# Kernel tuning notes

Hardware: AMD Instinct MI355X
Metric: run time of the kernel (lower is better)

## Reference

```python
import jax, jax.numpy as jnp
import numpy as np

N_USER, N_MOVIE, E, H, L = 100000, 20000, 1000000, 64, 2
NEG_SLOPE = 0.2  # PyG GATv2Conv default negative_slope


def _rand_edges(k, n_src, n_dst, e):
    k1, k2 = jax.random.split(k)
    src = jax.random.randint(k1, (e,), 0, n_src, dtype=jnp.int32)
    dst = jax.random.randint(k2, (e,), 0, n_dst, dtype=jnp.int32)
    # ensure no src==dst index collisions so PyG's remove_self_loops is a no-op
    dst = jnp.where(dst == src, (dst + 1) % n_dst, dst)
    return jnp.stack([src, dst])


def setup_inputs() -> dict:
    key = jax.random.key(0)
    ks = jax.random.split(key, 8)
    return {
        "x_user": jax.random.normal(ks[0], (N_USER, H), jnp.float32),
        "x_movie": jax.random.normal(ks[1], (N_MOVIE, H), jnp.float32),
        "edge_u2m": _rand_edges(ks[2], N_USER, N_MOVIE, E),
        "edge_m2u": _rand_edges(ks[3], N_MOVIE, N_USER, E),
        # params stacked as [layer, edge_type, ...]; edge_type 0 = user->movie, 1 = movie->user
        "Wl": jax.random.normal(ks[4], (L, 2, H, H), jnp.float32) / np.sqrt(H).astype(np.float32),
        "bl": jnp.zeros((L, 2, H), jnp.float32),
        "Wr": jax.random.normal(ks[5], (L, 2, H, H), jnp.float32) / np.sqrt(H).astype(np.float32),
        "br": jnp.zeros((L, 2, H), jnp.float32),
        "att": jax.random.normal(ks[6], (L, 2, H), jnp.float32) / np.sqrt(H).astype(np.float32),
        "bias": jnp.zeros((L, 2, H), jnp.float32),
    }


def _segment_softmax(scores, seg, n):
    # numerically-stable softmax over variable-degree dst neighborhoods (PyG softmax)
    m = jax.ops.segment_max(scores, seg, num_segments=n)
    ex = jnp.exp(scores - m[seg])
    s = jax.ops.segment_sum(ex, seg, num_segments=n)
    return ex / (s[seg] + 1e-16)


def _gatv2(x_src, x_dst, edge, Wl, bl, Wr, br, att, bias):
    n_src, n_dst = x_src.shape[0], x_dst.shape[0]
    xl = x_src @ Wl + bl  # [N_src, H]
    xr = x_dst @ Wr + br  # [N_dst, H]
    n_loop = min(n_src, n_dst)  # PyG adds self loops with num_nodes = min(N_src, N_dst)
    loop = jnp.arange(n_loop, dtype=edge.dtype)
    src = jnp.concatenate([edge[0], loop])
    dst = jnp.concatenate([edge[1], loop])
    e = jax.nn.leaky_relu(xl[src] + xr[dst], NEG_SLOPE)  # [E', H] gathered per edge
    score = e @ att  # [E']
    alpha = _segment_softmax(score, dst, n_dst)
    out = jax.ops.segment_sum(xl[src] * alpha[:, None], dst, num_segments=n_dst)
    return out + bias


def reference(x_user, x_movie, edge_u2m, edge_m2u, Wl, bl, Wr, br, att, bias):
    for l in range(L):
        new_movie = _gatv2(x_user, x_movie, edge_u2m,
                           Wl[l, 0], bl[l, 0], Wr[l, 0], br[l, 0], att[l, 0], bias[l, 0])
        new_user = _gatv2(x_movie, x_user, edge_m2u,
                          Wl[l, 1], bl[l, 1], Wr[l, 1], br[l, 1], att[l, 1], bias[l, 1])
        x_movie = jax.nn.selu(new_movie)
        x_user = jax.nn.selu(new_user)
    return x_user, x_movie
```

## Files before the change

kernel.cpp:

```cpp
#include <hip/hip_runtime.h>
#include <hip/hip_fp16.h>
#include <cstdint>

#define H 64
#define EPR 16
#define NB 120

__device__ __forceinline__ float selu_f(float x) {
  const float sc = 1.0507009873554805f;
  const float al = 1.6732632423543772f;
  return x > 0.f ? sc * x : sc * al * (expf(x) - 1.f);
}

__global__ __launch_bounds__(256) void gemm64_dual2(
    const float* __restrict__ Au, const float* __restrict__ Am,
    const float* __restrict__ W0u, const float* __restrict__ b0u,
    const float* __restrict__ W1u, const float* __restrict__ b1u,
    const float* __restrict__ W0m, const float* __restrict__ b0m,
    const float* __restrict__ W1m, const float* __restrict__ b1m,
    __half* __restrict__ C0u, float* __restrict__ C1u,
    __half* __restrict__ C0m, float* __restrict__ C1m,
    int Nu, int Nm, int split) {
  __shared__ float Ws0[64 * 64];
  __shared__ float Ws1[64 * 64];
  __shared__ float As[64][65];
  __shared__ float bs0[64], bs1[64];

  const float *A, *W0, *b0, *W1, *b1;
  __half* C0; float* C1; int N, blk;
  if (blockIdx.x < split) {
    A = Au; W0 = W0u; b0 = b0u; W1 = W1u; b1 = b1u;
    C0 = C0u; C1 = C1u; N = Nu; blk = blockIdx.x;
  } else {
    A = Am; W0 = W0m; b0 = b0m; W1 = W1m; b1 = b1m;
    C0 = C0m; C1 = C1m; N = Nm; blk = blockIdx.x - split;
  }

  const int tid = threadIdx.x;
  for (int i = tid; i < 1024; i += 256) {
    ((float4*)Ws0)[i] = ((const float4*)W0)[i];
    ((float4*)Ws1)[i] = ((const float4*)W1)[i];
  }
  if (tid < 64) { bs0[tid] = b0[tid]; bs1[tid] = b1[tid]; }

  const int row0 = blk * 64;
  for (int i = tid; i < 1024; i += 256) {
    int r = i >> 4, c4 = i & 15;
    int row = row0 + r;
    float4 v = make_float4(0.f, 0.f, 0.f, 0.f);
    if (row < N) v = ((const float4*)(A + (size_t)row * H))[c4];
    As[r][c4 * 4 + 0] = v.x;
    As[r][c4 * 4 + 1] = v.y;
    As[r][c4 * 4 + 2] = v.z;
    As[r][c4 * 4 + 3] = v.w;
  }
  __syncthreads();

  const int g = tid & 3;
  const int r = tid >> 2;
  float a0[16], a1[16];
#pragma unroll
  for (int j = 0; j < 16; ++j) { a0[j] = bs0[g * 16 + j]; a1[j] = bs1[g * 16 + j]; }

  for (int k = 0; k < 64; ++k) {
    float ak = As[r][k];
    const float4* w0r = (const float4*)&Ws0[k * 64 + g * 16];
    const float4* w1r = (const float4*)&Ws1[k * 64 + g * 16];
#pragma unroll
    for (int j4 = 0; j4 < 4; ++j4) {
      float4 w0 = w0r[j4], w1 = w1r[j4];
      a0[j4 * 4 + 0] += ak * w0.x; a0[j4 * 4 + 1] += ak * w0.y;
      a0[j4 * 4 + 2] += ak * w0.z; a0[j4 * 4 + 3] += ak * w0.w;
      a1[j4 * 4 + 0] += ak * w1.x; a1[j4 * 4 + 1] += ak * w1.y;
      a1[j4 * 4 + 2] += ak * w1.z; a1[j4 * 4 + 3] += ak * w1.w;
    }
  }

  const int row = row0 + r;
  if (row < N) {
    unsigned pu[8];
#pragma unroll
    for (int j2 = 0; j2 < 8; ++j2) {
      __half2 t = __floats2half2_rn(a0[2 * j2], a0[2 * j2 + 1]);
      pu[j2] = *(unsigned*)&t;
    }
    uint4* c0 = (uint4*)(C0 + (size_t)row * H + g * 16);
    c0[0] = make_uint4(pu[0], pu[1], pu[2], pu[3]);
    c0[1] = make_uint4(pu[4], pu[5], pu[6], pu[7]);

    float4* c1 = (float4*)(C1 + (size_t)row * H + g * 16);
#pragma unroll
    for (int j4 = 0; j4 < 4; ++j4) {
      c1[j4] = make_float4(a1[j4 * 4 + 0], a1[j4 * 4 + 1], a1[j4 * 4 + 2], a1[j4 * 4 + 3]);
    }
  }
}

__global__ __launch_bounds__(256) void bucket_hist(
    const int* __restrict__ ed1, int E1r, int n1e, int sh1, int B1, int* __restrict__ mat1,
    const int* __restrict__ ed2, int E2r, int n2e, int sh2, int B2, int* __restrict__ mat2) {
  __shared__ int hist[640];
  int b = blockIdx.x;
  const int* ed; int Er, ne, sh, Bn, blk; int* mat;
  if (b < NB) { ed = ed1; Er = E1r; ne = n1e; sh = sh1; Bn = B1; mat = mat1; blk = b; }
  else { ed = ed2; Er = E2r; ne = n2e; sh = sh2; Bn = B2; mat = mat2; blk = b - NB; }
  for (int i = threadIdx.x; i < Bn; i += 256) hist[i] = 0;
  __syncthreads();
  int chunk = (ne + NB - 1) / NB;
  int lo = blk * chunk, hi = lo + chunk;
  if (hi > ne) hi = ne;
  for (int e = lo + threadIdx.x; e < hi; e += 256) {
    int d = (e < Er) ? ed[e] : (e - Er);
    atomicAdd(&hist[d >> sh], 1);
  }
  __syncthreads();
  for (int i = threadIdx.x; i < Bn; i += 256) mat[(size_t)i * NB + blk] = hist[i];
}

__global__ __launch_bounds__(256) void scan_partial2(
    const int* __restrict__ cnt1, int n1, int* __restrict__ psum1, int* __restrict__ bsum1,
    const int* __restrict__ cnt2, int n2, int* __restrict__ psum2, int* __restrict__ bsum2,
    int split) {
  __shared__ int sh[256];
  int b = blockIdx.x;
  const int* cnt; int n; int* psum; int* bsum; int lb;
  if (b < split) { cnt = cnt1; n = n1; psum = psum1; bsum = bsum1; lb = b; }
  else { cnt = cnt2; n = n2; psum = psum2; bsum = bsum2; lb = b - split; }
  int i = lb * 256 + threadIdx.x;
  int tid = threadIdx.x;
  sh[tid] = (i < n) ? cnt[i] : 0;
  __syncthreads();
  for (int off = 1; off < 256; off <<= 1) {
    int t = (tid >= off) ? sh[tid - off] : 0;
    __syncthreads();
    if (tid >= off) sh[tid] += t;
    __syncthreads();
  }
  if (i < n) psum[i] = sh[tid];
  if (tid == 255) bsum[lb] = sh[255];
}

__global__ __launch_bounds__(256) void scan_bsums2(
    int* __restrict__ bsum1, int nb1, int* __restrict__ bsum2, int nb2) {
  __shared__ int sh[256];
  const int tid = threadIdx.x;
  for (int which = 0; which < 2; ++which) {
    int* bsum = which ? bsum2 : bsum1;
    int nb = which ? nb2 : nb1;
    int run = 0;
    for (int start = 0; start < nb; start += 256) {
      int i = start + tid;
      int v = (i < nb) ? bsum[i] : 0;
      __syncthreads();
      sh[tid] = v;
      __syncthreads();
      for (int off = 1; off < 256; off <<= 1) {
        int t = (tid >= off) ? sh[tid - off] : 0;
        __syncthreads();
        if (tid >= off) sh[tid] += t;
        __syncthreads();
      }
      if (i < nb) bsum[i] = run + sh[tid] - v;
      run += sh[255];
      __syncthreads();
    }
  }
}

__global__ __launch_bounds__(256) void finalize_excl2(
    const int* __restrict__ cnt1, const int* __restrict__ psum1,
    const int* __restrict__ bsum1, int n1, int* __restrict__ excl1,
    const int* __restrict__ cnt2, const int* __restrict__ psum2,
    const int* __restrict__ bsum2, int n2, int* __restrict__ excl2, int split) {
  int b = blockIdx.x;
  const int *cnt, *psum, *bsum; int n; int* excl; int lb;
  if (b < split) { cnt = cnt1; psum = psum1; bsum = bsum1; n = n1; excl = excl1; lb = b; }
  else { cnt = cnt2; psum = psum2; bsum = bsum2; n = n2; excl = excl2; lb = b - split; }
  int i = lb * 256 + threadIdx.x;
  if (i >= n) return;
  excl[i] = psum[i] + bsum[lb] - cnt[i];
}

__global__ __launch_bounds__(256) void bucket_part(
    const int* __restrict__ es1, const int* __restrict__ ed1, int E1r, int n1e,
    int sh1, int B1, const int* __restrict__ excl1, unsigned* __restrict__ part1,
    const int* __restrict__ es2, const int* __restrict__ ed2, int E2r, int n2e,
    int sh2, int B2, const int* __restrict__ excl2, unsigned* __restrict__ part2) {
  __shared__ int cur[640];
  int b = blockIdx.x;
  const int *es, *ed, *excl; int Er, ne, sh, Bn, blk; unsigned* part;
  if (b < NB) { es = es1; ed = ed1; Er = E1r; ne = n1e; sh = sh1; Bn = B1; excl = excl1; part = part1; blk = b; }
  else { es = es2; ed = ed2; Er = E2r; ne = n2e; sh = sh2; Bn = B2; excl = excl2; part = part2; blk = b - NB; }
  for (int i = threadIdx.x; i < Bn; i += 256) cur[i] = excl[(size_t)i * NB + blk];
  __syncthreads();
  int chunk = (ne + NB - 1) / NB;
  int lo = blk * chunk, hi = lo + chunk;
  if (hi > ne) hi = ne;
  const unsigned lmask = (1u << sh) - 1u;
  for (int e = lo + threadIdx.x; e < hi; e += 256) {
    int s, d;
    if (e < Er) { s = es[e]; d = ed[e]; } else { s = e - Er; d = s; }
    int bkt = d >> sh;
    int pos = atomicAdd(&cur[bkt], 1);
    part[pos] = (((unsigned)d & lmask) << 18) | (unsigned)s;
  }
}

__global__ __launch_bounds__(256) void bucket_sort(
    const unsigned* __restrict__ part1, const int* __restrict__ excl1,
    int n1e, int sh1, int B1, int nd1, int* __restrict__ rp1, int* __restrict__ csr1,
    const unsigned* __restrict__ part2, const int* __restrict__ excl2,
    int n2e, int sh2, int B2, int nd2, int* __restrict__ rp2, int* __restrict__ csr2) {
  __shared__ int cnt_s[256];
  __shared__ int scan_s[256];
  int b = blockIdx.x;
  const unsigned* part; const int* excl; int ne, sh, Bn, nd, bkt; int *rp, *csr;
  if (b < B1) { part = part1; excl = excl1; ne = n1e; sh = sh1; Bn = B1; nd = nd1; rp = rp1; csr = csr1; bkt = b; }
  else { part = part2; excl = excl2; ne = n2e; sh = sh2; Bn = B2; nd = nd2; rp = rp2; csr = csr2; bkt = b - B1; }
  const int tid = threadIdx.x;
  const int dbase = bkt << sh;
  const int R = 1 << sh;
  int rcap = nd - dbase;
  if (rcap > R) rcap = R;
  const int base = excl[(size_t)bkt * NB];
  const int endv = (bkt == Bn - 1) ? ne : excl[(size_t)(bkt + 1) * NB];

  cnt_s[tid] = 0;
  __syncthreads();
  for (int i = base + tid; i < endv; i += 256)
    atomicAdd(&cnt_s[part[i] >> 18], 1);
  __syncthreads();
  int c = cnt_s[tid];
  scan_s[tid] = c;
  __syncthreads();
  for (int off = 1; off < 256; off <<= 1) {
    int t = (tid >= off) ? scan_s[tid - off] : 0;
    __syncthreads();
    if (tid >= off) scan_s[tid] += t;
    __syncthreads();
  }
  if (tid < rcap) rp[dbase + tid + 1] = base + scan_s[tid];
  cnt_s[tid] = base + scan_s[tid] - c;
  if (tid == 0 && bkt == 0) rp[0] = 0;
  __syncthreads();
  for (int i = base + tid; i < endv; i += 256) {
    unsigned p = part[i];
    int dl = p >> 18;
    int pos = atomicAdd(&cnt_s[dl], 1);
    csr[pos] = (int)(p & 0x3FFFFu);
  }
}

__global__ __launch_bounds__(256) void gat_dst2(
    const int* __restrict__ rp1, const int* __restrict__ csr1,
    const __half* __restrict__ xl1, const float* __restrict__ xr1,
    const float* __restrict__ att1, const float* __restrict__ bias1,
    float* __restrict__ out1, int nd1,
    const int* __restrict__ rp2, const int* __restrict__ csr2,
    const __half* __restrict__ xl2, const float* __restrict__ xr2,
    const float* __restrict__ att2, const float* __restrict__ bias2,
    float* __restrict__ out2, int nd2, int split) {
  __shared__ __align__(16) float tile[4][EPR * 64];

  const int b = blockIdx.x;
  const int* rp; const int* csr; const __half* xl; const float *xr, *att, *bias;
  float* out; int nd, d0;
  if (b < split) {
    rp = rp1; csr = csr1; xl = xl1; xr = xr1; att = att1; bias = bias1;
    out = out1; nd = nd1; d0 = b * 4;
  } else {
    rp = rp2; csr = csr2; xl = xl2; xr = xr2; att = att2; bias = bias2;
    out = out2; nd = nd2; d0 = (b - split) * 4;
  }
  const int w = threadIdx.x >> 6;
  const int d = d0 + w;
  if (d >= nd) return;
  const int h = threadIdx.x & 63;
  const unsigned h2 = (unsigned)h * 2u;
  const char* xlb = (const char*)xl;
  float* tl = tile[w];

  const float xr_h = xr[(size_t)d * H + h];
  const float a = att[h];
  const float a06 = 0.6f * a, a04 = 0.4f * a;
  const float bias_h = bias[h];
  const int sbeg = __builtin_amdgcn_readfirstlane(rp[d]);
  const int send = __builtin_amdgcn_readfirstlane(rp[d + 1]);

  const int r = h & 15;
  const int q = h >> 4;
  const int pr = (q << 2) ^ r;

  float o;

  if (send - sbeg <= EPR) {
    const int cnt = send - sbeg;
    const int* csw = csr + sbeg;
    float v[EPR];
#pragma unroll
    for (int qq = 0; qq < EPR / 4; ++qq) {
      if (qq * 4 < cnt) {
#pragma unroll
        for (int i = 0; i < 4; ++i) {
          const int k = qq * 4 + i;
          int j = k < cnt ? k : cnt - 1;
          unsigned src = (unsigned)csw[j];
          v[k] = __half2float(*(const __half*)(xlb + ((src << 7) | h2)));
        }
      }
    }
#pragma unroll
    for (int qq = 0; qq < EPR / 4; ++qq) {
      if (qq * 4 < cnt) {
#pragma unroll
        for (int i = 0; i < 4; ++i) {
          const int k = qq * 4 + i;
          float p = v[k] + xr_h;
          tl[(k << 6) | (h ^ (k << 2))] = fmaf(p, a06, fabsf(p) * a04);
        }
      }
    }
    const float4* t4 = (const float4*)tl;
    float t0 = 0.f, t1 = 0.f, t2 = 0.f, t3 = 0.f;
#pragma unroll
    for (int c = 0; c < 4; ++c) {
      float4 q4 = t4[(r << 4) | (pr ^ c)];
      t0 += q4.x; t1 += q4.y; t2 += q4.z; t3 += q4.w;
    }
    float t = (t0 + t1) + (t2 + t3);
    t += __shfl_xor(t, 16, 64);
    t += __shfl_xor(t, 32, 64);
    t = (r < cnt) ? t : -3.0e38f;

    float M = t;
#pragma unroll
    for (int mk = 1; mk <= 8; mk <<= 1) M = fmaxf(M, __shfl_xor(M, mk, 64));
    float e = __expf(t - M);
    float S = e;
#pragma unroll
    for (int mk = 1; mk <= 8; mk <<= 1) S += __shfl_xor(S, mk, 64);
    if (h < 16) tl[h] = e;

    float P = 0.f;
#pragma unroll
    for (int qq = 0; qq < EPR / 4; ++qq) {
      if (qq * 4 < cnt) {
        float4 w4 = ((const float4*)tl)[qq];
        P += w4.x * v[qq * 4 + 0];
        P += w4.y * v[qq * 4 + 1];
        P += w4.z * v[qq * 4 + 2];
        P += w4.w * v[qq * 4 + 3];
      }
    }
    o = P / (S + 1e-16f) + bias_h;
  } else {
    float m = -3.0e38f, s = 0.f, acc = 0.f;
    int base = sbeg;
    float v[EPR], v2[EPR];

    {
      const int* csw = csr + base;
#pragma unroll
      for (int k = 0; k < EPR; ++k) {
        unsigned src = (unsigned)csw[k];
        v[k] = __half2float(*(const __half*)(xlb + ((src << 7) | h2)));
      }
    }

    auto round = [&](float (&vc)[EPR], float (&vp)[EPR]) -> bool {
      int cnt = send - base;
      if (cnt > EPR) cnt = EPR;
#pragma unroll
      for (int qq = 0; qq < EPR / 4; ++qq) {
        if (qq * 4 < cnt) {
#pragma unroll
          for (int i = 0; i < 4; ++i) {
            const int k = qq * 4 + i;
            float p = vc[k] + xr_h;
            tl[(k << 6) | (h ^ (k << 2))] = fmaf(p, a06, fabsf(p) * a04);
          }
        }
      }
      const int nbase = base + EPR;
      int ncnt = send - nbase;
      const bool have_next = ncnt > 0;
      if (ncnt > EPR) ncnt = EPR;
      if (have_next) {
        const int* csn = csr + nbase;
#pragma unroll
        for (int qq = 0; qq < EPR / 4; ++qq) {
          if (qq * 4 < ncnt) {
#pragma unroll
            for (int i = 0; i < 4; ++i) {
              const int k = qq * 4 + i;
              int j = k < ncnt ? k : ncnt - 1;
              unsigned src = (unsigned)csn[j];
              vp[k] = __half2float(*(const __half*)(xlb + ((src << 7) | h2)));
            }
          }
        }
      }
      const float4* t4 = (const float4*)tl;
      float t0 = 0.f, t1 = 0.f, t2 = 0.f, t3 = 0.f;
#pragma unroll
      for (int c = 0; c < 4; ++c) {
        float4 q4 = t4[(r << 4) | (pr ^ c)];
        t0 += q4.x; t1 += q4.y; t2 += q4.z; t3 += q4.w;
      }
      float t = (t0 + t1) + (t2 + t3);
      t += __shfl_xor(t, 16, 64);
      t += __shfl_xor(t, 32, 64);
      t = (r < cnt) ? t : -3.0e38f;

      float M = t;
#pragma unroll
      for (int mk = 1; mk <= 8; mk <<= 1) M = fmaxf(M, __shfl_xor(M, mk, 64));
      float e = __expf(t - M);
      float S = e;
#pragma unroll
      for (int mk = 1; mk <= 8; mk <<= 1) S += __shfl_xor(S, mk, 64);
      if (h < 16) tl[h] = e;

      float nm = fmaxf(m, M);
      float a_old = __expf(m - nm);
      float a_new = __expf(M - nm);
      float P = 0.f;
#pragma unroll
      for (int qq = 0; qq < EPR / 4; ++qq) {
        if (qq * 4 < cnt) {
          float4 w4 = ((const float4*)tl)[qq];
          P += w4.x * vc[qq * 4 + 0];
          P += w4.y * vc[qq * 4 + 1];
          P += w4.z * vc[qq * 4 + 2];
          P += w4.w * vc[qq * 4 + 3];
        }
      }
      s = s * a_old + S * a_new;
      acc = acc * a_old + P * a_new;
      m = nm;
      base = nbase;
      return have_next;
    };

    for (;;) {
      if (!round(v, v2)) break;
      if (!round(v2, v)) break;
    }
    o = acc / (s + 1e-16f) + bias_h;
  }

  out[(size_t)d * H + h] = selu_f(o);
}

extern "C" void kernel_launch(void* const* d_in, const int* in_sizes, int n_in,
                              void* d_out, int out_size, void* d_ws, size_t ws_size,
                              hipStream_t stream) {
  const float* x_user = (const float*)d_in[0];
  const float* x_movie = (const float*)d_in[1];
  const int* e_u2m = (const int*)d_in[2];
  const int* e_m2u = (const int*)d_in[3];
  const float* Wl = (const float*)d_in[4];
  const float* bl = (const float*)d_in[5];
  const float* Wr = (const float*)d_in[6];
  const float* br = (const float*)d_in[7];
  const float* att = (const float*)d_in[8];
  const float* bias = (const float*)d_in[9];

  const int n_user = in_sizes[0] / H;
  const int n_movie = in_sizes[1] / H;
  const int E1 = in_sizes[2] / 2;
  const int E2 = in_sizes[3] / 2;
  const int n_loop = n_user < n_movie ? n_user : n_movie;
  const int nE1 = E1 + n_loop;
  const int nE2 = E2 + n_loop;

  const int SHM = 5, SHU = 8;
  const int Bm = (n_movie + (1 << SHM) - 1) >> SHM;
  const int Bu = (n_user + (1 << SHU) - 1) >> SHU;
  const int nmatM = Bm * NB, nmatU = Bu * NB;
  const int nbm = (nmatM + 255) / 256, nbu = (nmatU + 255) / 256;

  float* ws = (float*)d_ws;
  size_t o = 0;
  __half* xl_u2m = (__half*)(ws + o); o += (size_t)n_user * H / 2;
  __half* xl_m2u = (__half*)(ws + o); o += (size_t)n_movie * H / 2;
  float* xr_u2m = ws + o; o += (size_t)n_movie * H;
  float* xr_m2u = ws + o; o += (size_t)n_user * H;

  int* matM  = (int*)(ws + o); o += nmatM;
  int* psumM = (int*)(ws + o); o += nmatM;
  int* exclM = (int*)(ws + o); o += nmatM;
  int* matU  = (int*)(ws + o); o += nmatU;
  int* psumU = (int*)(ws + o); o += nmatU;
  int* exclU = (int*)(ws + o); o += nmatU;
  int* bsumM = (int*)(ws + o); o += 1024;
  int* bsumU = (int*)(ws + o); o += 1024;
  unsigned* partM = (unsigned*)(ws + o); o += nE1;
  unsigned* partU = (unsigned*)(ws + o); o += nE2;
  int* csr1 = (int*)(ws + o); o += nE1;
  int* csr2 = (int*)(ws + o); o += nE2;
  int* rp1  = (int*)(ws + o); o += n_movie + 1;
  int* rp2  = (int*)(ws + o); o += n_user + 1;

  float* out_u = (float*)d_out;
  float* out_m = out_u + (size_t)n_user * H;

  const int gu = (n_user + 63) / 64;
  const int gm = (n_movie + 63) / 64;
  const int split1 = (n_movie + 3) / 4;
  const int split2 = (n_user + 3) / 4;

  bucket_hist<<<2 * NB, 256, 0, stream>>>(
      e_u2m + E1, E1, nE1, SHM, Bm, matM,
      e_m2u + E2, E2, nE2, SHU, Bu, matU);
  scan_partial2<<<nbm + nbu, 256, 0, stream>>>(
      matM, nmatM, psumM, bsumM, matU, nmatU, psumU, bsumU, nbm);
  scan_bsums2<<<1, 256, 0, stream>>>(bsumM, nbm, bsumU, nbu);
  finalize_excl2<<<nbm + nbu, 256, 0, stream>>>(
      matM, psumM, bsumM, nmatM, exclM,
      matU, psumU, bsumU, nmatU, exclU, nbm);
  bucket_part<<<2 * NB, 256, 0, stream>>>(
      e_u2m, e_u2m + E1, E1, nE1, SHM, Bm, exclM, partM,
      e_m2u, e_m2u + E2, E2, nE2, SHU, Bu, exclU, partU);
  bucket_sort<<<Bm + Bu, 256, 0, stream>>>(
      partM, exclM, nE1, SHM, Bm, n_movie, rp1, csr1,
      partU, exclU, nE2, SHU, Bu, n_user, rp2, csr2);

  for (int l = 0; l < 2; ++l) {
    const float* cu = (l == 0) ? x_user : out_u;
    const float* cm = (l == 0) ? x_movie : out_m;
    const int p0 = l * 2 + 0;
    const int p1 = l * 2 + 1;

    gemm64_dual2<<<gu + gm, 256, 0, stream>>>(
        cu, cm,
        Wl + (size_t)p0 * H * H, bl + (size_t)p0 * H,
        Wr + (size_t)p1 * H * H, br + (size_t)p1 * H,
        Wl + (size_t)p1 * H * H, bl + (size_t)p1 * H,
        Wr + (size_t)p0 * H * H, br + (size_t)p0 * H,
        xl_u2m, xr_m2u, xl_m2u, xr_u2m,
        n_user, n_movie, gu);

    gat_dst2<<<split1 + split2, 256, 0, stream>>>(
        rp1, csr1, xl_u2m, xr_u2m, att + (size_t)p0 * H, bias + (size_t)p0 * H,
        out_m, n_movie,
        rp2, csr2, xl_m2u, xr_m2u, att + (size_t)p1 * H, bias + (size_t)p1 * H,
        out_u, n_user, split1);
  }
}
```

Measured before the change: 440.8 us.

## Remap GAT aggregation lanes to edge×feature-quarter with vectorized half gathers

Rewrites the per-destination attention kernel so each lane handles one edge (16 edges) and a quarter of the features (16 halves). It gathers those halves with two 128-bit loads instead of one 2-byte load per lane per edge. Scores are computed in registers without the shared-memory tile. Per-feature outputs are accumulated per lane and then reduced across the 16 edge lanes with a butterfly transpose-reduce shuffle sequence. It also adds a launch-bounds occupancy hint, at the cost of more registers per thread (acc, v, v2, xr, att arrays).

```diff
diff --git a/kernel.cpp b/kernel.cpp
--- a/kernel.cpp
+++ b/kernel.cpp
@@ -251,7 +251,7 @@
   }
 }
 
-__global__ __launch_bounds__(256) void gat_dst2(
+__global__ __launch_bounds__(256, 4) void gat_dst4(
     const int* __restrict__ rp1, const int* __restrict__ csr1,
     const __half* __restrict__ xl1, const float* __restrict__ xr1,
     const float* __restrict__ att1, const float* __restrict__ bias1,
@@ -260,8 +260,6 @@
     const __half* __restrict__ xl2, const float* __restrict__ xr2,
     const float* __restrict__ att2, const float* __restrict__ bias2,
     float* __restrict__ out2, int nd2, int split) {
-  __shared__ __align__(16) float tile[4][EPR * 64];
-
   const int b = blockIdx.x;
   const int* rp; const int* csr; const __half* xl; const float *xr, *att, *bias;
   float* out; int nd, d0;
@@ -275,168 +273,145 @@
   const int w = threadIdx.x >> 6;
   const int d = d0 + w;
   if (d >= nd) return;
-  const int h = threadIdx.x & 63;
-  const unsigned h2 = (unsigned)h * 2u;
-  const char* xlb = (const char*)xl;
-  float* tl = tile[w];
-
-  const float xr_h = xr[(size_t)d * H + h];
-  const float a = att[h];
-  const float a06 = 0.6f * a, a04 = 0.4f * a;
-  const float bias_h = bias[h];
+  const int l = threadIdx.x & 63;
+  const int k = l & 15;
+  const int q = l >> 4;
+  const int brev = ((k & 1) << 3) | ((k & 2) << 1) | ((k & 4) >> 1) | ((k & 8) >> 3);
+  const int fout = q * 16 + brev;
+
+  float attv[16];
+  {
+    const float4* a4 = (const float4*)(att + q * 16);
+#pragma unroll
+    for (int i = 0; i < 4; ++i) {
+      float4 t = a4[i];
+      attv[4 * i + 0] = t.x; attv[4 * i + 1] = t.y;
+      attv[4 * i + 2] = t.z; attv[4 * i + 3] = t.w;
+    }
+  }
+  const float bias_o = bias[fout];
+
   const int sbeg = __builtin_amdgcn_readfirstlane(rp[d]);
   const int send = __builtin_amdgcn_readfirstlane(rp[d + 1]);
-
-  const int r = h & 15;
-  const int q = h >> 4;
-  const int pr = (q << 2) ^ r;
-
-  float o;
-
-  if (send - sbeg <= EPR) {
-    const int cnt = send - sbeg;
-    const int* csw = csr + sbeg;
-    float v[EPR];
-#pragma unroll
-    for (int qq = 0; qq < EPR / 4; ++qq) {
-      if (qq * 4 < cnt) {
-#pragma unroll
-        for (int i = 0; i < 4; ++i) {
-          const int k = qq * 4 + i;
-          int j = k < cnt ? k : cnt - 1;
-          unsigned src = (unsigned)csw[j];
-          v[k] = __half2float(*(const __half*)(xlb + ((src << 7) | h2)));
-        }
-      }
-    }
-#pragma unroll
-    for (int qq = 0; qq < EPR / 4; ++qq) {
-      if (qq * 4 < cnt) {
-#pragma unroll
-        for (int i = 0; i < 4; ++i) {
-          const int k = qq * 4 + i;
-          float p = v[k] + xr_h;
-          tl[(k << 6) | (h ^ (k << 2))] = fmaf(p, a06, fabsf(p) * a04);
-        }
-      }
-    }
-    const float4* t4 = (const float4*)tl;
-    float t0 = 0.f, t1 = 0.f, t2 = 0.f, t3 = 0.f;
-#pragma unroll
-    for (int c = 0; c < 4; ++c) {
-      float4 q4 = t4[(r << 4) | (pr ^ c)];
-      t0 += q4.x; t1 += q4.y; t2 += q4.z; t3 += q4.w;
-    }
-    float t = (t0 + t1) + (t2 + t3);
-    t += __shfl_xor(t, 16, 64);
-    t += __shfl_xor(t, 32, 64);
-    t = (r < cnt) ? t : -3.0e38f;
-
-    float M = t;
+  const int cnt_all = send - sbeg;
+
+  if (cnt_all <= 0) {
+    out[(size_t)d * H + l] = selu_f(bias[l]);
+    return;
+  }
+
+  float xrv[16];
+  {
+    const float4* x4 = (const float4*)(xr + (size_t)d * H + q * 16);
+#pragma unroll
+    for (int i = 0; i < 4; ++i) {
+      float4 t = x4[i];
+      xrv[4 * i + 0] = t.x; xrv[4 * i + 1] = t.y;
+      xrv[4 * i + 2] = t.z; xrv[4 * i + 3] = t.w;
+    }
+  }
+
+  const char* xlb = (const char*)xl;
+  const unsigned qb = (unsigned)q * 32u;
+  const int last = send - 1;
+
+  auto gather = [&](int basek, float (&v)[16]) {
+    int idx = basek + k;
+    if (idx > last) idx = last;
+    unsigned src = (unsigned)csr[idx];
+    const uint4* p = (const uint4*)(xlb + (((size_t)src) << 7) + qb);
+    uint4 u0 = p[0];
+    uint4 u1 = p[1];
+    unsigned uu[8] = {u0.x, u0.y, u0.z, u0.w, u1.x, u1.y, u1.z, u1.w};
+#pragma unroll
+    for (int i = 0; i < 8; ++i) {
+      __half2 hh = *(__half2*)&uu[i];
+      float2 f = __half22float2(hh);
+      v[2 * i + 0] = f.x;
+      v[2 * i + 1] = f.y;
+    }
+  };
+
+  float acc[16];
+  float denom;
+
+  if (cnt_all <= EPR) {
+    float v[16];
+    gather(sbeg, v);
+    float sa0 = 0.f, sa1 = 0.f, sa2 = 0.f, sa3 = 0.f;
+#pragma unroll
+    for (int j = 0; j < 16; j += 4) {
+      float p0 = v[j + 0] + xrv[j + 0];
+      float p1 = v[j + 1] + xrv[j + 1];
+      float p2 = v[j + 2] + xrv[j + 2];
+      float p3 = v[j + 3] + xrv[j + 3];
+      sa0 = fmaf(fmaf(p0, 0.6f, fabsf(p0) * 0.4f), attv[j + 0], sa0);
+      sa1 = fmaf(fmaf(p1, 0.6f, fabsf(p1) * 0.4f), attv[j + 1], sa1);
+      sa2 = fmaf(fmaf(p2, 0.6f, fabsf(p2) * 0.4f), attv[j + 2], sa2);
+      sa3 = fmaf(fmaf(p3, 0.6f, fabsf(p3) * 0.4f), attv[j + 3], sa3);
+    }
+    float sc = (sa0 + sa1) + (sa2 + sa3);
+    sc += __shfl_xor(sc, 16, 64);
+    sc += __shfl_xor(sc, 32, 64);
+    sc = (k < cnt_all) ? sc : -3.0e38f;
+
+    float M = sc;
 #pragma unroll
     for (int mk = 1; mk <= 8; mk <<= 1) M = fmaxf(M, __shfl_xor(M, mk, 64));
-    float e = __expf(t - M);
+    float e = __expf(sc - M);
     float S = e;
 #pragma unroll
     for (int mk = 1; mk <= 8; mk <<= 1) S += __shfl_xor(S, mk, 64);
-    if (h < 16) tl[h] = e;
-
-    float P = 0.f;
-#pragma unroll
-    for (int qq = 0; qq < EPR / 4; ++qq) {
-      if (qq * 4 < cnt) {
-        float4 w4 = ((const float4*)tl)[qq];
-        P += w4.x * v[qq * 4 + 0];
-        P += w4.y * v[qq * 4 + 1];
-        P += w4.z * v[qq * 4 + 2];
-        P += w4.w * v[qq * 4 + 3];
-      }
-    }
-    o = P / (S + 1e-16f) + bias_h;
+#pragma unroll
+    for (int j = 0; j < 16; ++j) acc[j] = e * v[j];
+    denom = S;
   } else {
-    float m = -3.0e38f, s = 0.f, acc = 0.f;
+    float m = -3.0e38f, s = 0.f;
+#pragma unroll
+    for (int j = 0; j < 16; ++j) acc[j] = 0.f;
+    float v[16], v2[16];
+    gather(sbeg, v);
     int base = sbeg;
-    float v[EPR], v2[EPR];
-
-    {
-      const int* csw = csr + base;
-#pragma unroll
-      for (int k = 0; k < EPR; ++k) {
-        unsigned src = (unsigned)csw[k];
-        v[k] = __half2float(*(const __half*)(xlb + ((src << 7) | h2)));
-      }
-    }
-
-    auto round = [&](float (&vc)[EPR], float (&vp)[EPR]) -> bool {
+
+    auto round = [&](float (&vc)[16], float (&vp)[16]) -> bool {
       int cnt = send - base;
       if (cnt > EPR) cnt = EPR;
-#pragma unroll
-      for (int qq = 0; qq < EPR / 4; ++qq) {
-        if (qq * 4 < cnt) {
-#pragma unroll
-          for (int i = 0; i < 4; ++i) {
-            const int k = qq * 4 + i;
-            float p = vc[k] + xr_h;
-            tl[(k << 6) | (h ^ (k << 2))] = fmaf(p, a06, fabsf(p) * a04);
-          }
-        }
+      float sa0 = 0.f, sa1 = 0.f, sa2 = 0.f, sa3 = 0.f;
+#pragma unroll
+      for (int j = 0; j < 16; j += 4) {
+        float p0 = vc[j + 0] + xrv[j + 0];
+        float p1 = vc[j + 1] + xrv[j + 1];
+        float p2 = vc[j + 2] + xrv[j + 2];
+        float p3 = vc[j + 3] + xrv[j + 3];
+        sa0 = fmaf(fmaf(p0, 0.6f, fabsf(p0) * 0.4f), attv[j + 0], sa0);
+        sa1 = fmaf(fmaf(p1, 0.6f, fabsf(p1) * 0.4f), attv[j + 1], sa1);
+        sa2 = fmaf(fmaf(p2, 0.6f, fabsf(p2) * 0.4f), attv[j + 2], sa2);
+        sa3 = fmaf(fmaf(p3, 0.6f, fabsf(p3) * 0.4f), attv[j + 3], sa3);
       }
       const int nbase = base + EPR;
-      int ncnt = send - nbase;
-      const bool have_next = ncnt > 0;
-      if (ncnt > EPR) ncnt = EPR;
-      if (have_next) {
-        const int* csn = csr + nbase;
-#pragma unroll
-        for (int qq = 0; qq < EPR / 4; ++qq) {
-          if (qq * 4 < ncnt) {
-#pragma unroll
-            for (int i = 0; i < 4; ++i) {
-              const int k = qq * 4 + i;
-              int j = k < ncnt ? k : ncnt - 1;
-              unsigned src = (unsigned)csn[j];
-              vp[k] = __half2float(*(const __half*)(xlb + ((src << 7) | h2)));
-            }
-          }
-        }
-      }
-      const float4* t4 = (const float4*)tl;
-      float t0 = 0.f, t1 = 0.f, t2 = 0.f, t3 = 0.f;
-#pragma unroll
-      for (int c = 0; c < 4; ++c) {
-        float4 q4 = t4[(r << 4) | (pr ^ c)];
-        t0 += q4.x; t1 += q4.y; t2 += q4.z; t3 += q4.w;
-      }
-      float t = (t0 + t1) + (t2 + t3);
-      t += __shfl_xor(t, 16, 64);
-      t += __shfl_xor(t, 32, 64);
-      t = (r < cnt) ? t : -3.0e38f;
-
-      float M = t;
+      const bool have_next = nbase < send;
+      if (have_next) gather(nbase, vp);
+
+      float sc = (sa0 + sa1) + (sa2 + sa3);
+      sc += __shfl_xor(sc, 16, 64);
+      sc += __shfl_xor(sc, 32, 64);
+      sc = (k < cnt) ? sc : -3.0e38f;
+
+      float M = sc;
 #pragma unroll
       for (int mk = 1; mk <= 8; mk <<= 1) M = fmaxf(M, __shfl_xor(M, mk, 64));
-      float e = __expf(t - M);
+      float e = __expf(sc - M);
       float S = e;
 #pragma unroll
       for (int mk = 1; mk <= 8; mk <<= 1) S += __shfl_xor(S, mk, 64);
-      if (h < 16) tl[h] = e;
 
       float nm = fmaxf(m, M);
       float a_old = __expf(m - nm);
       float a_new = __expf(M - nm);
-      float P = 0.f;
-#pragma unroll
-      for (int qq = 0; qq < EPR / 4; ++qq) {
-        if (qq * 4 < cnt) {
-          float4 w4 = ((const float4*)tl)[qq];
-          P += w4.x * vc[qq * 4 + 0];
-          P += w4.y * vc[qq * 4 + 1];
-          P += w4.z * vc[qq * 4 + 2];
-          P += w4.w * vc[qq * 4 + 3];
-        }
-      }
-      s = s * a_old + S * a_new;
-      acc = acc * a_old + P * a_new;
+      s = fmaf(s, a_old, S * a_new);
+      float ea = e * a_new;
+#pragma unroll
+      for (int j = 0; j < 16; ++j) acc[j] = fmaf(acc[j], a_old, ea * vc[j]);
       m = nm;
       base = nbase;
       return have_next;
@@ -446,10 +421,43 @@
       if (!round(v, v2)) break;
       if (!round(v2, v)) break;
     }
-    o = acc / (s + 1e-16f) + bias_h;
-  }
-
-  out[(size_t)d * H + h] = selu_f(o);
+    denom = s;
+  }
+
+  float r8[8];
+#pragma unroll
+  for (int i = 0; i < 8; ++i) {
+    float sendv = (k & 1) ? acc[i] : acc[i + 8];
+    float recv = __shfl_xor(sendv, 1, 64);
+    float keep = (k & 1) ? acc[i + 8] : acc[i];
+    r8[i] = keep + recv;
+  }
+  float r4[4];
+#pragma unroll
+  for (int i = 0; i < 4; ++i) {
+    float sendv = (k & 2) ? r8[i] : r8[i + 4];
+    float recv = __shfl_xor(sendv, 2, 64);
+    float keep = (k & 2) ? r8[i + 4] : r8[i];
+    r4[i] = keep + recv;
+  }
+  float r2[2];
+#pragma unroll
+  for (int i = 0; i < 2; ++i) {
+    float sendv = (k & 4) ? r4[i] : r4[i + 2];
+    float recv = __shfl_xor(sendv, 4, 64);
+    float keep = (k & 4) ? r4[i + 2] : r4[i];
+    r2[i] = keep + recv;
+  }
+  float r1;
+  {
+    float sendv = (k & 8) ? r2[0] : r2[1];
+    float recv = __shfl_xor(sendv, 8, 64);
+    float keep = (k & 8) ? r2[1] : r2[0];
+    r1 = keep + recv;
+  }
+
+  float o = r1 / (denom + 1e-16f) + bias_o;
+  out[(size_t)d * H + fout] = selu_f(o);
 }
 
 extern "C" void kernel_launch(void* const* d_in, const int* in_sizes, int n_in,
@@ -541,7 +549,7 @@
         xl_u2m, xr_m2u, xl_m2u, xr_u2m,
         n_user, n_movie, gu);
 
-    gat_dst2<<<split1 + split2, 256, 0, stream>>>(
+    gat_dst4<<<split1 + split2, 256, 0, stream>>>(
         rp1, csr1, xl_u2m, xr_u2m, att + (size_t)p0 * H, bias + (size_t)p0 * H,
         out_m, n_movie,
         rp2, csr2, xl_m2u, xr_m2u, att + (size_t)p1 * H, bias + (size_t)p1 * H,
```

After: 754.4 us. 1.71x slower.

## Split dual GEMM into per-weight blocks with 4-row register tiling

Applied to the files above, without the earlier changes.

The node projection GEMM now launches one block per (input, weight matrix) pair instead of computing both weight products in one block. Each 128-thread block handles 128 rows, with each thread keeping 4 rows by 16 columns of accumulators. A operands are read directly from global memory into registers, so the shared A tile is gone and each weight read from shared memory is reused across 4 rows. The input rows are now read twice (once per weight matrix), and the larger register footprint may lower occupancy.

```diff
diff --git a/kernel.cpp b/kernel.cpp
--- a/kernel.cpp
+++ b/kernel.cpp
@@ -12,7 +12,7 @@
   return x > 0.f ? sc * x : sc * al * (expf(x) - 1.f);
 }
 
-__global__ __launch_bounds__(256) void gemm64_dual2(
+__global__ __launch_bounds__(128) void gemm64_quad(
     const float* __restrict__ Au, const float* __restrict__ Am,
     const float* __restrict__ W0u, const float* __restrict__ b0u,
     const float* __restrict__ W1u, const float* __restrict__ b1u,
@@ -20,78 +20,92 @@
     const float* __restrict__ W1m, const float* __restrict__ b1m,
     __half* __restrict__ C0u, float* __restrict__ C1u,
     __half* __restrict__ C0m, float* __restrict__ C1m,
-    int Nu, int Nm, int split) {
-  __shared__ float Ws0[64 * 64];
-  __shared__ float Ws1[64 * 64];
-  __shared__ float As[64][65];
-  __shared__ float bs0[64], bs1[64];
-
-  const float *A, *W0, *b0, *W1, *b1;
-  __half* C0; float* C1; int N, blk;
-  if (blockIdx.x < split) {
-    A = Au; W0 = W0u; b0 = b0u; W1 = W1u; b1 = b1u;
-    C0 = C0u; C1 = C1u; N = Nu; blk = blockIdx.x;
-  } else {
-    A = Am; W0 = W0m; b0 = b0m; W1 = W1m; b1 = b1m;
-    C0 = C0m; C1 = C1m; N = Nm; blk = blockIdx.x - split;
-  }
+    int Nu, int Nm, int su, int sm) {
+  __shared__ float Ws[64 * 64];
+  __shared__ float bs[64];
+
+  const int b = blockIdx.x;
+  const float *A, *W, *bias; __half* Ch = nullptr; float* Cf = nullptr;
+  int N, blk; bool half_out;
+  if (b < su)            { A = Au; W = W0u; bias = b0u; Ch = C0u; N = Nu; blk = b;            half_out = true; }
+  else if (b < 2 * su)   { A = Au; W = W1u; bias = b1u; Cf = C1u; N = Nu; blk = b - su;       half_out = false; }
+  else if (b < 2*su+sm)  { A = Am; W = W0m; bias = b0m; Ch = C0m; N = Nm; blk = b - 2*su;     half_out = true; }
+  else                   { A = Am; W = W1m; bias = b1m; Cf = C1m; N = Nm; blk = b - 2*su - sm; half_out = false; }
 
   const int tid = threadIdx.x;
-  for (int i = tid; i < 1024; i += 256) {
-    ((float4*)Ws0)[i] = ((const float4*)W0)[i];
-    ((float4*)Ws1)[i] = ((const float4*)W1)[i];
-  }
-  if (tid < 64) { bs0[tid] = b0[tid]; bs1[tid] = b1[tid]; }
-
-  const int row0 = blk * 64;
-  for (int i = tid; i < 1024; i += 256) {
-    int r = i >> 4, c4 = i & 15;
-    int row = row0 + r;
-    float4 v = make_float4(0.f, 0.f, 0.f, 0.f);
-    if (row < N) v = ((const float4*)(A + (size_t)row * H))[c4];
-    As[r][c4 * 4 + 0] = v.x;
-    As[r][c4 * 4 + 1] = v.y;
-    As[r][c4 * 4 + 2] = v.z;
-    As[r][c4 * 4 + 3] = v.w;
-  }
+  for (int i = tid; i < 1024; i += 128) ((float4*)Ws)[i] = ((const float4*)W)[i];
+  if (tid < 64) bs[tid] = bias[tid];
   __syncthreads();
 
   const int g = tid & 3;
-  const int r = tid >> 2;
-  float a0[16], a1[16];
-#pragma unroll
-  for (int j = 0; j < 16; ++j) { a0[j] = bs0[g * 16 + j]; a1[j] = bs1[g * 16 + j]; }
-
-  for (int k = 0; k < 64; ++k) {
-    float ak = As[r][k];
-    const float4* w0r = (const float4*)&Ws0[k * 64 + g * 16];
-    const float4* w1r = (const float4*)&Ws1[k * 64 + g * 16];
-#pragma unroll
-    for (int j4 = 0; j4 < 4; ++j4) {
-      float4 w0 = w0r[j4], w1 = w1r[j4];
-      a0[j4 * 4 + 0] += ak * w0.x; a0[j4 * 4 + 1] += ak * w0.y;
-      a0[j4 * 4 + 2] += ak * w0.z; a0[j4 * 4 + 3] += ak * w0.w;
-      a1[j4 * 4 + 0] += ak * w1.x; a1[j4 * 4 + 1] += ak * w1.y;
-      a1[j4 * 4 + 2] += ak * w1.z; a1[j4 * 4 + 3] += ak * w1.w;
-    }
-  }
-
-  const int row = row0 + r;
-  if (row < N) {
-    unsigned pu[8];
-#pragma unroll
-    for (int j2 = 0; j2 < 8; ++j2) {
-      __half2 t = __floats2half2_rn(a0[2 * j2], a0[2 * j2 + 1]);
-      pu[j2] = *(unsigned*)&t;
-    }
-    uint4* c0 = (uint4*)(C0 + (size_t)row * H + g * 16);
-    c0[0] = make_uint4(pu[0], pu[1], pu[2], pu[3]);
-    c0[1] = make_uint4(pu[4], pu[5], pu[6], pu[7]);
-
-    float4* c1 = (float4*)(C1 + (size_t)row * H + g * 16);
-#pragma unroll
-    for (int j4 = 0; j4 < 4; ++j4) {
-      c1[j4] = make_float4(a1[j4 * 4 + 0], a1[j4 * 4 + 1], a1[j4 * 4 + 2], a1[j4 * 4 + 3]);
+  const int tr = tid >> 2;
+  const int row0 = blk * 128;
+
+  float acc[4][16];
+#pragma unroll
+  for (int i = 0; i < 4; ++i)
+#pragma unroll
+    for (int j = 0; j < 16; ++j) acc[i][j] = bs[g * 16 + j];
+
+  int rows[4]; int ar[4]; bool rok[4];
+#pragma unroll
+  for (int i = 0; i < 4; ++i) {
+    rows[i] = row0 + tr + 32 * i;
+    rok[i] = rows[i] < N;
+    ar[i] = rok[i] ? rows[i] : (N - 1);
+  }
+
+  for (int kt = 0; kt < 4; ++kt) {
+    float av[4][16];
+#pragma unroll
+    for (int i = 0; i < 4; ++i) {
+      const float4* ap = (const float4*)(A + (size_t)ar[i] * H + kt * 16);
+#pragma unroll
+      for (int c = 0; c < 4; ++c) {
+        float4 v = ap[c];
+        av[i][4 * c + 0] = v.x; av[i][4 * c + 1] = v.y;
+        av[i][4 * c + 2] = v.z; av[i][4 * c + 3] = v.w;
+      }
+    }
+#pragma unroll
+    for (int kk = 0; kk < 16; ++kk) {
+      const int k = kt * 16 + kk;
+      const float4* wr = (const float4*)&Ws[k * 64 + g * 16];
+      float w[16];
+#pragma unroll
+      for (int c = 0; c < 4; ++c) {
+        float4 t = wr[c];
+        w[4 * c + 0] = t.x; w[4 * c + 1] = t.y;
+        w[4 * c + 2] = t.z; w[4 * c + 3] = t.w;
+      }
+#pragma unroll
+      for (int i = 0; i < 4; ++i) {
+        float a = av[i][kk];
+#pragma unroll
+        for (int j = 0; j < 16; ++j) acc[i][j] = fmaf(a, w[j], acc[i][j]);
+      }
+    }
+  }
+
+#pragma unroll
+  for (int i = 0; i < 4; ++i) {
+    if (!rok[i]) continue;
+    if (half_out) {
+      unsigned pu[8];
+#pragma unroll
+      for (int j2 = 0; j2 < 8; ++j2) {
+        __half2 t = __floats2half2_rn(acc[i][2 * j2], acc[i][2 * j2 + 1]);
+        pu[j2] = *(unsigned*)&t;
+      }
+      uint4* c0 = (uint4*)(Ch + (size_t)rows[i] * H + g * 16);
+      c0[0] = make_uint4(pu[0], pu[1], pu[2], pu[3]);
+      c0[1] = make_uint4(pu[4], pu[5], pu[6], pu[7]);
+    } else {
+      float4* c1 = (float4*)(Cf + (size_t)rows[i] * H + g * 16);
+#pragma unroll
+      for (int c = 0; c < 4; ++c)
+        c1[c] = make_float4(acc[i][4 * c + 0], acc[i][4 * c + 1],
+                            acc[i][4 * c + 2], acc[i][4 * c + 3]);
     }
   }
 }
@@ -505,8 +519,8 @@
   float* out_u = (float*)d_out;
   float* out_m = out_u + (size_t)n_user * H;
 
-  const int gu = (n_user + 63) / 64;
-  const int gm = (n_movie + 63) / 64;
+  const int su = (n_user + 127) / 128;
+  const int sm = (n_movie + 127) / 128;
   const int split1 = (n_movie + 3) / 4;
   const int split2 = (n_user + 3) / 4;
 
@@ -532,14 +546,14 @@
     const int p0 = l * 2 + 0;
     const int p1 = l * 2 + 1;
 
-    gemm64_dual2<<<gu + gm, 256, 0, stream>>>(
+    gemm64_quad<<<2 * (su + sm), 128, 0, stream>>>(
         cu, cm,
         Wl + (size_t)p0 * H * H, bl + (size_t)p0 * H,
         Wr + (size_t)p1 * H * H, br + (size_t)p1 * H,
         Wl + (size_t)p1 * H * H, bl + (size_t)p1 * H,
         Wr + (size_t)p0 * H * H, br + (size_t)p0 * H,
         xl_u2m, xr_m2u, xl_m2u, xr_u2m,
-        n_user, n_movie, gu);
+        n_user, n_movie, su, sm);
 
     gat_dst2<<<split1 + split2, 256, 0, stream>>>(
         rp1, csr1, xl_u2m, xr_u2m, att + (size_t)p0 * H, bias + (size_t)p0 * H,
```

Result: slower. 469.0 us (+6.4%).
